# Optimization experiments

Hardware: AMD Instinct MI355X
Metric: run time of the kernel (lower is better)

Reference implementation:

```python
import jax, jax.numpy as jnp
import numpy as np

B, S, D = 4, 4096, 64

def setup_inputs() -> dict:
    key = jax.random.key(0)
    k1, k2 = jax.random.split(key)
    query = jax.random.normal(k1, (B, S, D), dtype=jnp.float32)
    value = jax.random.normal(k2, (B, S, D), dtype=jnp.float32)
    return {"query": query, "value": value}

def reference(query, value):
    # score = Q @ V^T  -> [B, Sq, Skv]  (note: value acts as both key and value; no 1/sqrt(d) scaling)
    score = jnp.einsum("bqd,bkd->bqk", query, value)
    attn_weights = jax.nn.softmax(score, axis=-1)
    context = jnp.einsum("bqk,bkd->bqd", attn_weights, value)
    return (context, attn_weights)
```

## Files before the change

### kernel.cpp

```cpp
#include <hip/hip_runtime.h>

#define BB 4
#define SS 4096
#define DD 64
#define QB 32
#define TK 64
#define SV 72
#define SP 72

typedef _Float16 h16;
typedef h16 half4_t __attribute__((ext_vector_type(4)));
typedef h16 half8_t __attribute__((ext_vector_type(8)));
typedef float f32x4 __attribute__((ext_vector_type(4)));

struct LdsBufs {
    h16 Vhi[2][TK * SV];
    h16 Vlo[2][TK * SV];
    h16 VTr[2][DD * SV];
    h16 Pl[4][16 * SP];
};

__device__ __forceinline__ void stage(LdsBufs& L, const float* Vb, int it, int t,
                                      bool with_vt) {
    const int ts  = t >> 7;
    const int tt  = t & 127;
    const int c16 = tt & 15;
    const int kr  = tt >> 4;
    const f32x4* Vg = (const f32x4*)(Vb + ((size_t)(it * 2 + ts) * TK + kr * 8) * DD);
    half4_t hh[8];
#pragma unroll
    for (int i = 0; i < 8; ++i) {
        f32x4 v = Vg[i * 16 + c16];
        half4_t hi, lo;
#pragma unroll
        for (int j = 0; j < 4; ++j) {
            float x = v[j];
            h16 h = (h16)x;
            hi[j] = h;
            lo[j] = (h16)(x - (float)h);
        }
        hh[i] = hi;
        *(half4_t*)&L.Vhi[ts][(kr * 8 + i) * SV + c16 * 4] = hi;
        *(half4_t*)&L.Vlo[ts][(kr * 8 + i) * SV + c16 * 4] = lo;
    }
    if (with_vt) {
#pragma unroll
        for (int j = 0; j < 4; ++j) {
            half8_t col;
#pragma unroll
            for (int i = 0; i < 8; ++i) col[i] = hh[i][j];
            *(half8_t*)&L.VTr[ts][(c16 * 4 + j) * SV + kr * 8] = col;
        }
    }
}

__device__ __forceinline__ void scores(const LdsBufs& L, int ts, int qi, int quad,
                                       const half8_t* qhi, const half8_t* qlo,
                                       f32x4* sc) {
#pragma unroll
    for (int mt = 0; mt < 4; ++mt) sc[mt] = (f32x4){0.f, 0.f, 0.f, 0.f};
#pragma unroll
    for (int ks = 0; ks < 2; ++ks) {
#pragma unroll
        for (int mt = 0; mt < 4; ++mt) {
            half8_t ahi = *(const half8_t*)&L.Vhi[ts][(mt * 16 + qi) * SV + ks * 32 + quad * 8];
            half8_t alo = *(const half8_t*)&L.Vlo[ts][(mt * 16 + qi) * SV + ks * 32 + quad * 8];
            sc[mt] = __builtin_amdgcn_mfma_f32_16x16x32_f16(ahi, qhi[ks], sc[mt], 0, 0, 0);
            sc[mt] = __builtin_amdgcn_mfma_f32_16x16x32_f16(ahi, qlo[ks], sc[mt], 0, 0, 0);
            sc[mt] = __builtin_amdgcn_mfma_f32_16x16x32_f16(alo, qhi[ks], sc[mt], 0, 0, 0);
        }
    }
}

__global__ __launch_bounds__(256, 2) void attn_fused(const float* __restrict__ Q,
                                                     const float* __restrict__ V,
                                                     float* __restrict__ ctx,
                                                     float* __restrict__ attn) {
    __shared__ LdsBufs L;
    const int t     = threadIdx.x;
    const int w     = t >> 6;
    const int lane  = t & 63;
    const int qi    = lane & 15;
    const int quad  = lane >> 4;
    const int qgrp  = w & 1;
    const int khalf = w >> 1;
    const int b     = blockIdx.y;
    const int qb    = blockIdx.x * QB + qgrp * 16;

    const float* Vb   = V + (size_t)b * SS * DD;
    const float* Qrow = Q + ((size_t)b * SS + qb + qi) * DD;

    half8_t qhi[2], qlo[2];
#pragma unroll
    for (int ks = 0; ks < 2; ++ks) {
        const float* p = Qrow + ks * 32 + quad * 8;
#pragma unroll
        for (int j = 0; j < 8; ++j) {
            float x = p[j];
            h16 h = (h16)x;
            qhi[ks][j] = h;
            qlo[ks][j] = (h16)(x - (float)h);
        }
    }

    float mrun = -1e30f, lrun = 0.f;
    f32x4 oc[4];
#pragma unroll
    for (int mt = 0; mt < 4; ++mt) oc[mt] = (f32x4){0.f, 0.f, 0.f, 0.f};

    for (int it = 0; it < SS / TK / 2; ++it) {
        __syncthreads();
        stage(L, Vb, it, t, true);
        __syncthreads();

        f32x4 sc[4];
        scores(L, khalf, qi, quad, qhi, qlo, sc);

        float tmax = -1e30f;
#pragma unroll
        for (int mt = 0; mt < 4; ++mt)
#pragma unroll
            for (int r = 0; r < 4; ++r) tmax = fmaxf(tmax, sc[mt][r]);
        tmax = fmaxf(tmax, __shfl_xor(tmax, 16));
        tmax = fmaxf(tmax, __shfl_xor(tmax, 32));
        float mn    = fmaxf(mrun, tmax);
        float alpha = __expf(mrun - mn);
        float psum  = 0.f;
        half4_t pv[4];
#pragma unroll
        for (int mt = 0; mt < 4; ++mt)
#pragma unroll
            for (int r = 0; r < 4; ++r) {
                float p = __expf(sc[mt][r] - mn);
                psum += p;
                pv[mt][r] = (h16)p;
            }
        psum += __shfl_xor(psum, 16);
        psum += __shfl_xor(psum, 32);
        lrun = lrun * alpha + psum;
        mrun = mn;
#pragma unroll
        for (int mt = 0; mt < 4; ++mt) {
            oc[mt] *= alpha;
            *(half4_t*)&L.Pl[w][qi * SP + mt * 16 + quad * 4] = pv[mt];
        }

#pragma unroll
        for (int ks = 0; ks < 2; ++ks) {
            half8_t bp = *(const half8_t*)&L.Pl[w][qi * SP + ks * 32 + quad * 8];
#pragma unroll
            for (int mt = 0; mt < 4; ++mt) {
                half8_t av = *(const half8_t*)&L.VTr[khalf][(mt * 16 + qi) * SV + ks * 32 + quad * 8];
                oc[mt] = __builtin_amdgcn_mfma_f32_16x16x32_f16(av, bp, oc[mt], 0, 0, 0);
            }
        }
    }

    __syncthreads();
    {
        float* buf  = (float*)&L.Vhi[0][0];
        float* mine = buf + (w * 64 + lane) * 18;
        mine[0] = mrun;
        mine[1] = lrun;
#pragma unroll
        for (int mt = 0; mt < 4; ++mt)
#pragma unroll
            for (int r = 0; r < 4; ++r) mine[2 + mt * 4 + r] = oc[mt][r];
        __syncthreads();
        const float* po = buf + ((w ^ 2) * 64 + lane) * 18;
        float m2 = po[0], l2 = po[1];
        float mn = fmaxf(mrun, m2);
        float ea = __expf(mrun - mn), eb = __expf(m2 - mn);
        lrun = lrun * ea + l2 * eb;
#pragma unroll
        for (int mt = 0; mt < 4; ++mt)
#pragma unroll
            for (int r = 0; r < 4; ++r)
                oc[mt][r] = oc[mt][r] * ea + po[2 + mt * 4 + r] * eb;
        mrun = mn;
    }

    const float invl = 1.f / lrun;

    if (khalf == 0) {
        float* crow = ctx + ((size_t)b * SS + qb + qi) * DD;
#pragma unroll
        for (int mt = 0; mt < 4; ++mt) {
            f32x4 cv;
#pragma unroll
            for (int r = 0; r < 4; ++r) cv[r] = oc[mt][r] * invl;
            *(f32x4*)&crow[mt * 16 + quad * 4] = cv;
        }
    }

    float* arow = attn + ((size_t)b * SS + qb + qi) * SS;
    for (int it = 0; it < SS / TK / 2; ++it) {
        __syncthreads();
        stage(L, Vb, it, t, false);
        __syncthreads();

        f32x4 sc[4];
        scores(L, khalf, qi, quad, qhi, qlo, sc);
        const int kt = it * 2 + khalf;
#pragma unroll
        for (int mt = 0; mt < 4; ++mt) {
            f32x4 wv;
#pragma unroll
            for (int r = 0; r < 4; ++r) wv[r] = __expf(sc[mt][r] - mrun) * invl;
            *(f32x4*)&arow[kt * TK + mt * 16 + quad * 4] = wv;
        }
    }
}

extern "C" void kernel_launch(void* const* d_in, const int* in_sizes, int n_in,
                              void* d_out, int out_size, void* d_ws, size_t ws_size,
                              hipStream_t stream) {
    const float* Q = (const float*)d_in[0];
    const float* V = (const float*)d_in[1];
    float* ctx  = (float*)d_out;
    float* attn = (float*)d_out + (size_t)BB * SS * DD;
    attn_fused<<<dim3(SS / QB, BB), 256, 0, stream>>>(Q, V, ctx, attn);
}
```

Before: 385.3 us.

## Split key dimension across eight waves and prefetch V tiles into registers

Doubles the block to 512 threads. Each of four key-quarter wave pairs processes a 32-key tile, so partial softmax states must be merged from four ways instead of two. The next V tile's global loads are issued into registers before the current tile's compute, overlapping load latency with MFMA work. The second pass folds normalisation into a single exp offset (m + log l), and Q loads are vectorised. This adds LDS pressure and a wider reduction, and its occupancy assumptions (launch_bounds 512,4) may limit registers.

```diff
diff --git a/kernel.cpp b/kernel.cpp
--- a/kernel.cpp
+++ b/kernel.cpp
@@ -4,8 +4,10 @@
 #define SS 4096
 #define DD 64
 #define QB 32
-#define TK 64
+#define TK 32
+#define NS 4
 #define SV 72
+#define SVT 40
 #define SP 72
 
 typedef _Float16 h16;
@@ -13,24 +15,33 @@
 typedef h16 half8_t __attribute__((ext_vector_type(8)));
 typedef float f32x4 __attribute__((ext_vector_type(4)));
 
-struct LdsBufs {
-    h16 Vhi[2][TK * SV];
-    h16 Vlo[2][TK * SV];
-    h16 VTr[2][DD * SV];
-    h16 Pl[4][16 * SP];
+struct __align__(16) LdsBufs {
+    h16 Vhi[NS][TK * SV];
+    h16 Vlo[NS][TK * SV];
+    h16 VTr[NS][DD * SVT];
+    h16 Pl[8][16 * SP];
 };
-
-__device__ __forceinline__ void stage(LdsBufs& L, const float* Vb, int it, int t,
-                                      bool with_vt) {
-    const int ts  = t >> 7;
-    const int tt  = t & 127;
-    const int c16 = tt & 15;
-    const int kr  = tt >> 4;
-    const f32x4* Vg = (const f32x4*)(Vb + ((size_t)(it * 2 + ts) * TK + kr * 8) * DD);
-    half4_t hh[8];
-#pragma unroll
-    for (int i = 0; i < 8; ++i) {
-        f32x4 v = Vg[i * 16 + c16];
+static_assert(sizeof(LdsBufs) <= 80 * 1024, "need 2 blocks/CU");
+
+struct StReg { f32x4 v[4]; };
+
+__device__ __forceinline__ void stage_load(StReg& r, const float* Vb, int it, int t) {
+    const int c16 = t & 15;
+    const int rg  = t >> 4;
+    const f32x4* Vg = (const f32x4*)(Vb + ((size_t)it * (NS * TK) + rg * 4) * DD);
+#pragma unroll
+    for (int i = 0; i < 4; ++i) r.v[i] = Vg[i * 16 + c16];
+}
+
+__device__ __forceinline__ void stage_write(const StReg& r, LdsBufs& L, int t, bool with_vt) {
+    const int c16 = t & 15;
+    const int rg  = t >> 4;
+    const int ts  = rg >> 3;
+    const int r0  = (rg & 7) * 4;
+    half4_t hh[4];
+#pragma unroll
+    for (int i = 0; i < 4; ++i) {
+        f32x4 v = r.v[i];
         half4_t hi, lo;
 #pragma unroll
         for (int j = 0; j < 4; ++j) {
@@ -40,31 +51,31 @@
             lo[j] = (h16)(x - (float)h);
         }
         hh[i] = hi;
-        *(half4_t*)&L.Vhi[ts][(kr * 8 + i) * SV + c16 * 4] = hi;
-        *(half4_t*)&L.Vlo[ts][(kr * 8 + i) * SV + c16 * 4] = lo;
+        *(half4_t*)&L.Vhi[ts][(r0 + i) * SV + c16 * 4] = hi;
+        *(half4_t*)&L.Vlo[ts][(r0 + i) * SV + c16 * 4] = lo;
     }
     if (with_vt) {
 #pragma unroll
         for (int j = 0; j < 4; ++j) {
-            half8_t col;
-#pragma unroll
-            for (int i = 0; i < 8; ++i) col[i] = hh[i][j];
-            *(half8_t*)&L.VTr[ts][(c16 * 4 + j) * SV + kr * 8] = col;
-        }
-    }
-}
-
-__device__ __forceinline__ void scores(const LdsBufs& L, int ts, int qi, int quad,
+            half4_t col;
+#pragma unroll
+            for (int i = 0; i < 4; ++i) col[i] = hh[i][j];
+            *(half4_t*)&L.VTr[ts][(c16 * 4 + j) * SVT + r0] = col;
+        }
+    }
+}
+
+__device__ __forceinline__ void scores(const LdsBufs& L, int kq, int qi, int quad,
                                        const half8_t* qhi, const half8_t* qlo,
                                        f32x4* sc) {
-#pragma unroll
-    for (int mt = 0; mt < 4; ++mt) sc[mt] = (f32x4){0.f, 0.f, 0.f, 0.f};
+    sc[0] = (f32x4){0.f, 0.f, 0.f, 0.f};
+    sc[1] = (f32x4){0.f, 0.f, 0.f, 0.f};
 #pragma unroll
     for (int ks = 0; ks < 2; ++ks) {
 #pragma unroll
-        for (int mt = 0; mt < 4; ++mt) {
-            half8_t ahi = *(const half8_t*)&L.Vhi[ts][(mt * 16 + qi) * SV + ks * 32 + quad * 8];
-            half8_t alo = *(const half8_t*)&L.Vlo[ts][(mt * 16 + qi) * SV + ks * 32 + quad * 8];
+        for (int mt = 0; mt < 2; ++mt) {
+            half8_t ahi = *(const half8_t*)&L.Vhi[kq][(mt * 16 + qi) * SV + ks * 32 + quad * 8];
+            half8_t alo = *(const half8_t*)&L.Vlo[kq][(mt * 16 + qi) * SV + ks * 32 + quad * 8];
             sc[mt] = __builtin_amdgcn_mfma_f32_16x16x32_f16(ahi, qhi[ks], sc[mt], 0, 0, 0);
             sc[mt] = __builtin_amdgcn_mfma_f32_16x16x32_f16(ahi, qlo[ks], sc[mt], 0, 0, 0);
             sc[mt] = __builtin_amdgcn_mfma_f32_16x16x32_f16(alo, qhi[ks], sc[mt], 0, 0, 0);
@@ -72,7 +83,7 @@
     }
 }
 
-__global__ __launch_bounds__(256, 2) void attn_fused(const float* __restrict__ Q,
+__global__ __launch_bounds__(512, 4) void attn_fused(const float* __restrict__ Q,
                                                      const float* __restrict__ V,
                                                      float* __restrict__ ctx,
                                                      float* __restrict__ attn) {
@@ -83,7 +94,7 @@
     const int qi    = lane & 15;
     const int quad  = lane >> 4;
     const int qgrp  = w & 1;
-    const int khalf = w >> 1;
+    const int kq    = w >> 1;
     const int b     = blockIdx.y;
     const int qb    = blockIdx.x * QB + qgrp * 16;
 
@@ -93,13 +104,18 @@
     half8_t qhi[2], qlo[2];
 #pragma unroll
     for (int ks = 0; ks < 2; ++ks) {
-        const float* p = Qrow + ks * 32 + quad * 8;
-#pragma unroll
-        for (int j = 0; j < 8; ++j) {
-            float x = p[j];
+        f32x4 a = *(const f32x4*)(Qrow + ks * 32 + quad * 8);
+        f32x4 c = *(const f32x4*)(Qrow + ks * 32 + quad * 8 + 4);
+#pragma unroll
+        for (int j = 0; j < 4; ++j) {
+            float x = a[j];
             h16 h = (h16)x;
             qhi[ks][j] = h;
             qlo[ks][j] = (h16)(x - (float)h);
+            float y = c[j];
+            h16 g = (h16)y;
+            qhi[ks][j + 4] = g;
+            qlo[ks][j + 4] = (h16)(y - (float)g);
         }
     }
 
@@ -108,106 +124,123 @@
 #pragma unroll
     for (int mt = 0; mt < 4; ++mt) oc[mt] = (f32x4){0.f, 0.f, 0.f, 0.f};
 
-    for (int it = 0; it < SS / TK / 2; ++it) {
-        __syncthreads();
-        stage(L, Vb, it, t, true);
-        __syncthreads();
-
-        f32x4 sc[4];
-        scores(L, khalf, qi, quad, qhi, qlo, sc);
+    const int NIT = SS / (NS * TK);
+    StReg r;
+    stage_load(r, Vb, 0, t);
+
+    for (int it = 0; it < NIT; ++it) {
+        __syncthreads();
+        stage_write(r, L, t, true);
+        __syncthreads();
+        if (it + 1 < NIT) stage_load(r, Vb, it + 1, t);
+
+        f32x4 sc[2];
+        scores(L, kq, qi, quad, qhi, qlo, sc);
 
         float tmax = -1e30f;
 #pragma unroll
-        for (int mt = 0; mt < 4; ++mt)
-#pragma unroll
-            for (int r = 0; r < 4; ++r) tmax = fmaxf(tmax, sc[mt][r]);
+        for (int mt = 0; mt < 2; ++mt)
+#pragma unroll
+            for (int r4 = 0; r4 < 4; ++r4) tmax = fmaxf(tmax, sc[mt][r4]);
         tmax = fmaxf(tmax, __shfl_xor(tmax, 16));
         tmax = fmaxf(tmax, __shfl_xor(tmax, 32));
         float mn    = fmaxf(mrun, tmax);
         float alpha = __expf(mrun - mn);
         float psum  = 0.f;
-        half4_t pv[4];
-#pragma unroll
-        for (int mt = 0; mt < 4; ++mt)
-#pragma unroll
-            for (int r = 0; r < 4; ++r) {
-                float p = __expf(sc[mt][r] - mn);
+        half4_t pv[2];
+#pragma unroll
+        for (int mt = 0; mt < 2; ++mt)
+#pragma unroll
+            for (int r4 = 0; r4 < 4; ++r4) {
+                float p = __expf(sc[mt][r4] - mn);
                 psum += p;
-                pv[mt][r] = (h16)p;
+                pv[mt][r4] = (h16)p;
             }
         psum += __shfl_xor(psum, 16);
         psum += __shfl_xor(psum, 32);
         lrun = lrun * alpha + psum;
         mrun = mn;
 #pragma unroll
+        for (int mt = 0; mt < 2; ++mt)
+            *(half4_t*)&L.Pl[w][qi * SP + mt * 16 + quad * 4] = pv[mt];
+#pragma unroll
+        for (int mt = 0; mt < 4; ++mt) oc[mt] *= alpha;
+
+        half8_t bp = *(const half8_t*)&L.Pl[w][qi * SP + quad * 8];
+#pragma unroll
         for (int mt = 0; mt < 4; ++mt) {
-            oc[mt] *= alpha;
-            *(half4_t*)&L.Pl[w][qi * SP + mt * 16 + quad * 4] = pv[mt];
-        }
-
-#pragma unroll
-        for (int ks = 0; ks < 2; ++ks) {
-            half8_t bp = *(const half8_t*)&L.Pl[w][qi * SP + ks * 32 + quad * 8];
-#pragma unroll
-            for (int mt = 0; mt < 4; ++mt) {
-                half8_t av = *(const half8_t*)&L.VTr[khalf][(mt * 16 + qi) * SV + ks * 32 + quad * 8];
-                oc[mt] = __builtin_amdgcn_mfma_f32_16x16x32_f16(av, bp, oc[mt], 0, 0, 0);
-            }
-        }
-    }
+            half8_t av = *(const half8_t*)&L.VTr[kq][(mt * 16 + qi) * SVT + quad * 8];
+            oc[mt] = __builtin_amdgcn_mfma_f32_16x16x32_f16(av, bp, oc[mt], 0, 0, 0);
+        }
+    }
+
+    stage_load(r, Vb, 0, t);
 
     __syncthreads();
     {
-        float* buf  = (float*)&L.Vhi[0][0];
-        float* mine = buf + (w * 64 + lane) * 18;
+        float* buf  = (float*)&L;
+        float* mine = buf + t * 18;
         mine[0] = mrun;
         mine[1] = lrun;
 #pragma unroll
         for (int mt = 0; mt < 4; ++mt)
 #pragma unroll
-            for (int r = 0; r < 4; ++r) mine[2 + mt * 4 + r] = oc[mt][r];
-        __syncthreads();
-        const float* po = buf + ((w ^ 2) * 64 + lane) * 18;
-        float m2 = po[0], l2 = po[1];
-        float mn = fmaxf(mrun, m2);
-        float ea = __expf(mrun - mn), eb = __expf(m2 - mn);
-        lrun = lrun * ea + l2 * eb;
-#pragma unroll
-        for (int mt = 0; mt < 4; ++mt)
-#pragma unroll
-            for (int r = 0; r < 4; ++r)
-                oc[mt][r] = oc[mt][r] * ea + po[2 + mt * 4 + r] * eb;
-        mrun = mn;
+            for (int r4 = 0; r4 < 4; ++r4) mine[2 + mt * 4 + r4] = oc[mt][r4];
+        __syncthreads();
+        float mf = -1e30f;
+#pragma unroll
+        for (int k2 = 0; k2 < 4; ++k2)
+            mf = fmaxf(mf, buf[((k2 * 2 + qgrp) * 64 + lane) * 18]);
+        float lf = 0.f;
+        f32x4 on[4];
+#pragma unroll
+        for (int mt = 0; mt < 4; ++mt) on[mt] = (f32x4){0.f, 0.f, 0.f, 0.f};
+#pragma unroll
+        for (int k2 = 0; k2 < 4; ++k2) {
+            const float* po = buf + ((k2 * 2 + qgrp) * 64 + lane) * 18;
+            float e = __expf(po[0] - mf);
+            lf += po[1] * e;
+#pragma unroll
+            for (int mt = 0; mt < 4; ++mt)
+#pragma unroll
+                for (int r4 = 0; r4 < 4; ++r4) on[mt][r4] += po[2 + mt * 4 + r4] * e;
+        }
+        mrun = mf;
+        lrun = lf;
+#pragma unroll
+        for (int mt = 0; mt < 4; ++mt) oc[mt] = on[mt];
     }
 
     const float invl = 1.f / lrun;
 
-    if (khalf == 0) {
+    if (kq == 0) {
         float* crow = ctx + ((size_t)b * SS + qb + qi) * DD;
 #pragma unroll
         for (int mt = 0; mt < 4; ++mt) {
             f32x4 cv;
 #pragma unroll
-            for (int r = 0; r < 4; ++r) cv[r] = oc[mt][r] * invl;
+            for (int r4 = 0; r4 < 4; ++r4) cv[r4] = oc[mt][r4] * invl;
             *(f32x4*)&crow[mt * 16 + quad * 4] = cv;
         }
     }
 
+    const float moff = mrun + __logf(lrun);
     float* arow = attn + ((size_t)b * SS + qb + qi) * SS;
-    for (int it = 0; it < SS / TK / 2; ++it) {
-        __syncthreads();
-        stage(L, Vb, it, t, false);
-        __syncthreads();
-
-        f32x4 sc[4];
-        scores(L, khalf, qi, quad, qhi, qlo, sc);
-        const int kt = it * 2 + khalf;
-#pragma unroll
-        for (int mt = 0; mt < 4; ++mt) {
+    for (int it = 0; it < NIT; ++it) {
+        __syncthreads();
+        stage_write(r, L, t, false);
+        __syncthreads();
+        if (it + 1 < NIT) stage_load(r, Vb, it + 1, t);
+
+        f32x4 sc[2];
+        scores(L, kq, qi, quad, qhi, qlo, sc);
+        const int kbase = it * (NS * TK) + kq * TK;
+#pragma unroll
+        for (int mt = 0; mt < 2; ++mt) {
             f32x4 wv;
 #pragma unroll
-            for (int r = 0; r < 4; ++r) wv[r] = __expf(sc[mt][r] - mrun) * invl;
-            *(f32x4*)&arow[kt * TK + mt * 16 + quad * 4] = wv;
+            for (int r4 = 0; r4 < 4; ++r4) wv[r4] = __expf(sc[mt][r4] - moff);
+            *(f32x4*)&arow[kbase + mt * 16 + quad * 4] = wv;
         }
     }
 }
@@ -219,5 +252,5 @@
     const float* V = (const float*)d_in[1];
     float* ctx  = (float*)d_out;
     float* attn = (float*)d_out + (size_t)BB * SS * DD;
-    attn_fused<<<dim3(SS / QB, BB), 256, 0, stream>>>(Q, V, ctx, attn);
-}
+    attn_fused<<<dim3(SS / QB, BB), 512, 0, stream>>>(Q, V, ctx, attn);
+}
```

After: 377.2 us. 1.02x faster.
